# Kernel optimization log

Measured on AMD Instinct MI355X. Metric: run time of the kernel, lower is better.

## Reference

```python
import jax, jax.numpy as jnp
import numpy as np

B, S, DIN, DOUT = 4, 2048, 4096, 4096

def setup_inputs() -> dict:
    key = jax.random.key(0)
    k1, k2, k3, k4 = jax.random.split(key, 4)
    x = jax.random.normal(k1, (B, S, DIN), dtype=jnp.float32)
    # int8-valued quantized weights in [-127, 127]
    weight_int8 = jax.random.randint(k2, (DOUT, DIN), -127, 128, dtype=jnp.int32).astype(jnp.int8)
    # per-output-row scales, positive, clamped at 1e-8 like the torch code
    weight_scale = jnp.maximum(jax.random.uniform(k3, (DOUT, 1), dtype=jnp.float32) * 0.01, 1e-8)
    bias = jax.random.normal(k4, (DOUT,), dtype=jnp.float32)
    return {"x": x, "weight_int8": weight_int8, "weight_scale": weight_scale, "bias": bias}

def reference(x, weight_int8, weight_scale, bias):
    # Dequantize: [DOUT, DIN] = int8 * per-row scale (broadcast over in_features)
    w = weight_int8.astype(x.dtype) * weight_scale.astype(x.dtype)
    # F.linear: y = x @ w.T + bias
    return jnp.einsum('bsd,od->bso', x, w) + bias
```

## Files before the change

kernel.cpp:

```cpp
#include <hip/hip_runtime.h>
#include <stdint.h>

#define MM 8192
#define NN 4096
#define KK 4096
#define BM 256
#define BN 256
#define BK 64
#define NT (KK / BK)

typedef short bf16x8 __attribute__((ext_vector_type(8)));
typedef float f32x4 __attribute__((ext_vector_type(4)));

__device__ __forceinline__ unsigned int f2bf(float f) {
    unsigned int u = __builtin_bit_cast(unsigned int, f);
    u += 0x7FFFu + ((u >> 16) & 1u);
    return u >> 16;
}

__global__ __launch_bounds__(256) void cvt_kernel(const float* __restrict__ x,
                                                  const int* __restrict__ w,
                                                  unsigned short* __restrict__ xb,
                                                  unsigned short* __restrict__ wb) {
    const int stride = gridDim.x * blockDim.x;
    const int tid0 = blockIdx.x * blockDim.x + threadIdx.x;
    const int nx = MM * KK / 4;
    for (int i = tid0; i < nx; i += stride) {
        float4 v = ((const float4*)x)[i];
        uint2 o;
        o.x = f2bf(v.x) | (f2bf(v.y) << 16);
        o.y = f2bf(v.z) | (f2bf(v.w) << 16);
        ((uint2*)xb)[i] = o;
    }
    const int nw = NN * KK / 4;
    for (int i = tid0; i < nw; i += stride) {
        int4 v = ((const int4*)w)[i];
        uint2 o;
        o.x = f2bf((float)v.x) | (f2bf((float)v.y) << 16);
        o.y = f2bf((float)v.z) | (f2bf((float)v.w) << 16);
        ((uint2*)wb)[i] = o;
    }
}

#define SWZ(q) ((q) ^ ((((q) >> 8) & 7) << 4))

__global__ __launch_bounds__(512, 2) void gemm_kernel(const unsigned short* __restrict__ A,
                                                      const unsigned short* __restrict__ Bt,
                                                      const float* __restrict__ scale,
                                                      const float* __restrict__ bias,
                                                      float* __restrict__ C) {
    __shared__ __align__(16) unsigned short As[2][BM * BK];
    __shared__ __align__(16) unsigned short Bs[2][BN * BK];

    const int nbn = NN / BN;
    const int cpx = ((MM / BM) * (NN / BN)) >> 3;
    int bid = blockIdx.x;
    int swzb = (bid & 7) * cpx + (bid >> 3);
    const int bm = swzb / nbn;
    const int bn = swzb % nbn;

    const int tid  = threadIdx.x;
    const int lane = tid & 63;
    const int wid  = tid >> 6;
    const int wm   = wid >> 2;
    const int wn   = wid & 3;
    const int r    = lane & 15;
    const int kg   = lane >> 4;

    const int rowA0 = bm * BM;
    const int rowB0 = bn * BN;

    const int rt0   = (r * 128 + kg * 16) ^ ((r >> 1) << 4);
    const int offA0 = wm * 8192 + rt0;
    const int offA1 = offA0 ^ 64;
    const int offB0 = wn * 4096 + rt0;
    const int offB1 = offB0 ^ 64;
    char* Ab = (char*)As;
    char* Bb = (char*)Bs;

    int goA[2][2], goB[2][2], lo[2][2];
#pragma unroll
    for (int hi = 0; hi < 2; ++hi)
#pragma unroll
        for (int ii = 0; ii < 2; ++ii) {
            int q  = (hi << 14) + (ii * 512 + tid) * 16;
            int qs = SWZ(q);
            int rw = qs >> 7, cb = qs & 127;
            goA[hi][ii] = (rowA0 + rw) * (KK * 2) + cb;
            goB[hi][ii] = (rowB0 + rw) * (KK * 2) + cb;
            lo[hi][ii]  = (hi << 14) + ii * 8192 + wid * 1024;
        }

    f32x4 acc[8][4] = {};
    bf16x8 a[4][2], b0[2][2], b1[2][2];

#define STAGE_A(hi_, tt_, BUFO_) do {                                             \
    if ((tt_) < NT) {                                                             \
        _Pragma("unroll")                                                         \
        for (int ii = 0; ii < 2; ++ii) {                                          \
            const char* gs = (const char*)A + goA[hi_][ii] + (tt_) * 128;         \
            char* ld = Ab + (BUFO_) + lo[hi_][ii];                                \
            __builtin_amdgcn_global_load_lds(                                     \
                (const __attribute__((address_space(1))) unsigned int*)gs,        \
                (__attribute__((address_space(3))) unsigned int*)ld, 16, 0, 0);   \
        }                                                                         \
    }                                                                             \
} while (0)

#define STAGE_B(hi_, tt_, BUFO_) do {                                             \
    if ((tt_) < NT) {                                                             \
        _Pragma("unroll")                                                         \
        for (int ii = 0; ii < 2; ++ii) {                                          \
            const char* gs = (const char*)Bt + goB[hi_][ii] + (tt_) * 128;        \
            char* ld = Bb + (BUFO_) + lo[hi_][ii];                                \
            __builtin_amdgcn_global_load_lds(                                     \
                (const __attribute__((address_space(1))) unsigned int*)gs,        \
                (__attribute__((address_space(3))) unsigned int*)ld, 16, 0, 0);   \
        }                                                                         \
    }                                                                             \
} while (0)

#define READ_A(mh_, BUFO_) do {                                                   \
    _Pragma("unroll")                                                             \
    for (int i_ = 0; i_ < 4; ++i_) {                                              \
        a[i_][0] = *(const bf16x8*)(Ab + (BUFO_) + (mh_) * 16384 + i_ * 2048 + offA0); \
        a[i_][1] = *(const bf16x8*)(Ab + (BUFO_) + (mh_) * 16384 + i_ * 2048 + offA1); \
    }                                                                             \
} while (0)

#define READ_B(nh_, dst_, BUFO_) do {                                             \
    _Pragma("unroll")                                                             \
    for (int j_ = 0; j_ < 2; ++j_) {                                              \
        dst_[j_][0] = *(const bf16x8*)(Bb + (BUFO_) + (nh_) * 16384 + j_ * 2048 + offB0); \
        dst_[j_][1] = *(const bf16x8*)(Bb + (BUFO_) + (nh_) * 16384 + j_ * 2048 + offB1); \
    }                                                                             \
} while (0)

#define MFMA_Q(mh_, nh_, B_) do {                                                 \
    _Pragma("unroll")                                                             \
    for (int s_ = 0; s_ < 2; ++s_)                                                \
        _Pragma("unroll")                                                         \
        for (int i_ = 0; i_ < 4; ++i_)                                            \
            _Pragma("unroll")                                                     \
            for (int j_ = 0; j_ < 2; ++j_)                                        \
                acc[(mh_) * 4 + i_][(nh_) * 2 + j_] =                             \
                    __builtin_amdgcn_mfma_f32_16x16x32_bf16(                      \
                        a[i_][s_], B_[j_][s_], acc[(mh_) * 4 + i_][(nh_) * 2 + j_], 0, 0, 0); \
} while (0)

#define KTILE(t_, BUFO_, OTHER_) do {                                             \
    READ_A(0, BUFO_);                                                             \
    READ_B(0, b0, BUFO_);                                                         \
    STAGE_A(1, (t_) + 1, OTHER_);                                                 \
    asm volatile("s_waitcnt lgkmcnt(8)");                                         \
    __builtin_amdgcn_s_barrier();                                                 \
    asm volatile("s_waitcnt lgkmcnt(0)");                                         \
    __builtin_amdgcn_s_setprio(1); MFMA_Q(0, 0, b0); __builtin_amdgcn_s_setprio(0); \
    __builtin_amdgcn_s_barrier();                                                 \
    READ_B(1, b1, BUFO_);                                                         \
    STAGE_A(0, (t_) + 2, BUFO_);                                                  \
    __builtin_amdgcn_s_barrier();                                                 \
    asm volatile("s_waitcnt lgkmcnt(0)");                                         \
    __builtin_amdgcn_s_setprio(1); MFMA_Q(0, 1, b1); __builtin_amdgcn_s_setprio(0); \
    __builtin_amdgcn_s_barrier();                                                 \
    READ_A(1, BUFO_);                                                             \
    STAGE_B(0, (t_) + 2, BUFO_);                                                  \
    __builtin_amdgcn_s_barrier();                                                 \
    asm volatile("s_waitcnt lgkmcnt(0)");                                         \
    __builtin_amdgcn_s_setprio(1); MFMA_Q(1, 1, b1); __builtin_amdgcn_s_setprio(0); \
    __builtin_amdgcn_s_barrier();                                                 \
    STAGE_B(1, (t_) + 2, BUFO_);                                                  \
    __builtin_amdgcn_s_barrier();                                                 \
    __builtin_amdgcn_s_setprio(1); MFMA_Q(1, 0, b0); __builtin_amdgcn_s_setprio(0); \
    if ((t_) < NT - 1) {                                                          \
        if ((t_) == NT - 2) asm volatile("s_waitcnt vmcnt(0)");                   \
        else                asm volatile("s_waitcnt vmcnt(6)");                   \
        __builtin_amdgcn_s_barrier();                                             \
    }                                                                             \
} while (0)

    STAGE_A(0, 0, 0);
    STAGE_B(0, 0, 0);
    STAGE_B(1, 0, 0);
    STAGE_A(1, 0, 0);
    asm volatile("s_waitcnt vmcnt(4)");
    STAGE_A(0, 1, 0x8000);
    STAGE_B(0, 1, 0x8000);
    STAGE_B(1, 1, 0x8000);
    asm volatile("s_waitcnt vmcnt(6)");
    __builtin_amdgcn_s_barrier();

    for (int t2 = 0; t2 < NT; t2 += 2) {
        KTILE(t2,     0,      0x8000);
        KTILE(t2 + 1, 0x8000, 0);
    }

    const int rj = lane >> 4;
#pragma unroll
    for (int nj = 0; nj < 4; ++nj) {
        int col  = bn * BN + (nj >> 1) * 128 + wn * 32 + (nj & 1) * 16 + r;
        float sc = scale[col];
        float bi = bias[col];
#pragma unroll
        for (int mi = 0; mi < 8; ++mi) {
            int row = bm * BM + (mi >> 2) * 128 + wm * 64 + (mi & 3) * 16 + rj * 4;
#pragma unroll
            for (int j = 0; j < 4; ++j) {
                C[(size_t)(row + j) * NN + col] = acc[mi][nj][j] * sc + bi;
            }
        }
    }
#undef STAGE_A
#undef STAGE_B
#undef READ_A
#undef READ_B
#undef MFMA_Q
#undef KTILE
}

extern "C" void kernel_launch(void* const* d_in, const int* in_sizes, int n_in,
                              void* d_out, int out_size, void* d_ws, size_t ws_size,
                              hipStream_t stream) {
    const float* x     = (const float*)d_in[0];
    const int*   w8    = (const int*)d_in[1];
    const float* scale = (const float*)d_in[2];
    const float* bias  = (const float*)d_in[3];
    float* out = (float*)d_out;

    unsigned short* xb = (unsigned short*)d_ws;
    unsigned short* wb = xb + (size_t)MM * KK;

    cvt_kernel<<<8192, 256, 0, stream>>>(x, w8, xb, wb);
    gemm_kernel<<<(MM / BM) * (NN / BN), 512, 0, stream>>>(xb, wb, scale, bias, out);
}
```

Measured before the change: 525.0 us.

## Software-pipeline LDS fragment reads across MFMA quadrants with double A registers

Splits the A fragment registers into low and high halves and reorders each K-tile so LDS reads for the next quadrant, including the first quadrant of the next tile, are issued before the current quadrant's MFMAs. This overlaps ds_read latency with matrix math and reduces the number of barriers per tile. sched_barrier calls pin the order, and the vmcnt and lgkmcnt waits are retuned. The cost is extra VGPRs for the second A buffer and more fragile wait counts, where an off-by-one would race on LDS.

```diff
diff --git a/kernel.cpp b/kernel.cpp
--- a/kernel.cpp
+++ b/kernel.cpp
@@ -92,7 +92,7 @@
         }
 
     f32x4 acc[8][4] = {};
-    bf16x8 a[4][2], b0[2][2], b1[2][2];
+    bf16x8 aL[4][2], aH[4][2], b0[2][2], b1[2][2];
 
 #define STAGE_A(hi_, tt_, BUFO_) do {                                             \
     if ((tt_) < NT) {                                                             \
@@ -120,15 +120,15 @@
     }                                                                             \
 } while (0)
 
-#define READ_A(mh_, BUFO_) do {                                                   \
+#define READ_A(dst_, mh_, BUFO_) do {                                             \
     _Pragma("unroll")                                                             \
     for (int i_ = 0; i_ < 4; ++i_) {                                              \
-        a[i_][0] = *(const bf16x8*)(Ab + (BUFO_) + (mh_) * 16384 + i_ * 2048 + offA0); \
-        a[i_][1] = *(const bf16x8*)(Ab + (BUFO_) + (mh_) * 16384 + i_ * 2048 + offA1); \
-    }                                                                             \
-} while (0)
-
-#define READ_B(nh_, dst_, BUFO_) do {                                             \
+        dst_[i_][0] = *(const bf16x8*)(Ab + (BUFO_) + (mh_) * 16384 + i_ * 2048 + offA0); \
+        dst_[i_][1] = *(const bf16x8*)(Ab + (BUFO_) + (mh_) * 16384 + i_ * 2048 + offA1); \
+    }                                                                             \
+} while (0)
+
+#define READ_B(dst_, nh_, BUFO_) do {                                             \
     _Pragma("unroll")                                                             \
     for (int j_ = 0; j_ < 2; ++j_) {                                              \
         dst_[j_][0] = *(const bf16x8*)(Bb + (BUFO_) + (nh_) * 16384 + j_ * 2048 + offB0); \
@@ -136,7 +136,7 @@
     }                                                                             \
 } while (0)
 
-#define MFMA_Q(mh_, nh_, B_) do {                                                 \
+#define MFMA_Q(mh_, nh_, A_, B_) do {                                             \
     _Pragma("unroll")                                                             \
     for (int s_ = 0; s_ < 2; ++s_)                                                \
         _Pragma("unroll")                                                         \
@@ -145,50 +145,58 @@
             for (int j_ = 0; j_ < 2; ++j_)                                        \
                 acc[(mh_) * 4 + i_][(nh_) * 2 + j_] =                             \
                     __builtin_amdgcn_mfma_f32_16x16x32_bf16(                      \
-                        a[i_][s_], B_[j_][s_], acc[(mh_) * 4 + i_][(nh_) * 2 + j_], 0, 0, 0); \
+                        A_[i_][s_], B_[j_][s_], acc[(mh_) * 4 + i_][(nh_) * 2 + j_], 0, 0, 0); \
 } while (0)
 
 #define KTILE(t_, BUFO_, OTHER_) do {                                             \
-    READ_A(0, BUFO_);                                                             \
-    READ_B(0, b0, BUFO_);                                                         \
+                    \
     STAGE_A(1, (t_) + 1, OTHER_);                                                 \
-    asm volatile("s_waitcnt lgkmcnt(8)");                                         \
-    __builtin_amdgcn_s_barrier();                                                 \
-    asm volatile("s_waitcnt lgkmcnt(0)");                                         \
-    __builtin_amdgcn_s_setprio(1); MFMA_Q(0, 0, b0); __builtin_amdgcn_s_setprio(0); \
-    __builtin_amdgcn_s_barrier();                                                 \
-    READ_B(1, b1, BUFO_);                                                         \
+    READ_B(b1, 1, BUFO_);                                                         \
+    asm volatile("s_waitcnt lgkmcnt(4)" ::: "memory");                            \
+    __builtin_amdgcn_sched_barrier(0);                                            \
+    __builtin_amdgcn_s_setprio(1); MFMA_Q(0, 0, aL, b0); __builtin_amdgcn_s_setprio(0); \
+    __builtin_amdgcn_sched_barrier(0);                                            \
+    __builtin_amdgcn_s_barrier();                                                 \
+                                \
     STAGE_A(0, (t_) + 2, BUFO_);                                                  \
-    __builtin_amdgcn_s_barrier();                                                 \
-    asm volatile("s_waitcnt lgkmcnt(0)");                                         \
-    __builtin_amdgcn_s_setprio(1); MFMA_Q(0, 1, b1); __builtin_amdgcn_s_setprio(0); \
-    __builtin_amdgcn_s_barrier();                                                 \
-    READ_A(1, BUFO_);                                                             \
+    READ_A(aH, 1, BUFO_);                                                         \
+    asm volatile("s_waitcnt lgkmcnt(8)" ::: "memory");                            \
+    __builtin_amdgcn_sched_barrier(0);                                            \
+    __builtin_amdgcn_s_setprio(1); MFMA_Q(0, 1, aL, b1); __builtin_amdgcn_s_setprio(0); \
+    __builtin_amdgcn_sched_barrier(0);                                            \
+    __builtin_amdgcn_s_barrier();                                                 \
+                   \
     STAGE_B(0, (t_) + 2, BUFO_);                                                  \
-    __builtin_amdgcn_s_barrier();                                                 \
-    asm volatile("s_waitcnt lgkmcnt(0)");                                         \
-    __builtin_amdgcn_s_setprio(1); MFMA_Q(1, 1, b1); __builtin_amdgcn_s_setprio(0); \
-    __builtin_amdgcn_s_barrier();                                                 \
+    asm volatile("s_waitcnt lgkmcnt(0)" ::: "memory");                            \
+    __builtin_amdgcn_sched_barrier(0);                                            \
+    __builtin_amdgcn_s_setprio(1); MFMA_Q(1, 0, aH, b0); __builtin_amdgcn_s_setprio(0); \
+    __builtin_amdgcn_sched_barrier(0);                                            \
+    if ((t_) == NT - 2)     asm volatile("s_waitcnt vmcnt(0)" ::: "memory");      \
+    else if ((t_) < NT - 2) asm volatile("s_waitcnt vmcnt(4)" ::: "memory");      \
+    __builtin_amdgcn_s_barrier();                                                 \
+                    \
     STAGE_B(1, (t_) + 2, BUFO_);                                                  \
-    __builtin_amdgcn_s_barrier();                                                 \
-    __builtin_amdgcn_s_setprio(1); MFMA_Q(1, 0, b0); __builtin_amdgcn_s_setprio(0); \
     if ((t_) < NT - 1) {                                                          \
-        if ((t_) == NT - 2) asm volatile("s_waitcnt vmcnt(0)");                   \
-        else                asm volatile("s_waitcnt vmcnt(6)");                   \
-        __builtin_amdgcn_s_barrier();                                             \
-    }                                                                             \
+        READ_A(aL, 0, OTHER_);                                                    \
+        READ_B(b0, 0, OTHER_);                                                    \
+    }                                                                             \
+    __builtin_amdgcn_sched_barrier(0);                                            \
+    __builtin_amdgcn_s_setprio(1); MFMA_Q(1, 1, aH, b1); __builtin_amdgcn_s_setprio(0); \
+    __builtin_amdgcn_sched_barrier(0);                                            \
+    __builtin_amdgcn_s_barrier();                                                 \
 } while (0)
 
     STAGE_A(0, 0, 0);
     STAGE_B(0, 0, 0);
     STAGE_B(1, 0, 0);
     STAGE_A(1, 0, 0);
-    asm volatile("s_waitcnt vmcnt(4)");
     STAGE_A(0, 1, 0x8000);
     STAGE_B(0, 1, 0x8000);
     STAGE_B(1, 1, 0x8000);
-    asm volatile("s_waitcnt vmcnt(6)");
+    asm volatile("s_waitcnt vmcnt(6)" ::: "memory");
     __builtin_amdgcn_s_barrier();
+    READ_A(aL, 0, 0);
+    READ_B(b0, 0, 0);
 
     for (int t2 = 0; t2 < NT; t2 += 2) {
         KTILE(t2,     0,      0x8000);
```

Result: slower. 605.3 us (+15.3%).
